# Kernel optimization log

Measured on AMD Instinct MI355X. Metric: run time of the kernel, lower is better.

The kernel has to match this reference:

```python
import jax, jax.numpy as jnp
import numpy as np

HEADS = 8
DIM_HEAD = 64

def setup_inputs() -> dict:
    key = jax.random.key(0)
    k1, k2, k3 = jax.random.split(key, 3)
    B, L, D = 8, 4096, 512
    hidden = HEADS * DIM_HEAD  # 512
    x = jax.random.normal(k1, (B, L, D), dtype=jnp.float32)
    # Conv1d(kernel_size=1) weights, squeezed to 2D matrices
    Wqkv = jax.random.normal(k2, (3 * hidden, D), dtype=jnp.float32) * (1.0 / np.sqrt(D))
    Wout = jax.random.normal(k3, (D, hidden), dtype=jnp.float32) * (1.0 / np.sqrt(hidden))
    bout = jnp.zeros((D,), dtype=jnp.float32)
    return {"x": x, "Wqkv": Wqkv, "Wout": Wout, "bout": bout}

def reference(x, Wqkv, Wout, bout):
    B, L, D = x.shape
    H, C = HEADS, DIM_HEAD
    # pointwise conv == linear over channel dim: (b, 3*H*C, l)
    qkv = jnp.einsum('bld,od->bol', x, Wqkv)
    qkv = qkv.reshape(B, 3, H, C, L)  # channel split order: (qkv, heads, c)
    q, k, v = qkv[:, 0], qkv[:, 1], qkv[:, 2]  # each (b, h, c, l)
    k = jax.nn.softmax(k, axis=-1)   # softmax over sequence
    q = jax.nn.softmax(q, axis=-2)   # softmax over feature dim (q_norm=True)
    context = jnp.einsum('bhdn,bhen->bhde', k, v)   # (b,h,c,c)
    out = jnp.einsum('bhde,bhdn->bhen', context, q)  # (b,h,c,l)
    out = out.reshape(B, H * C, L)
    y = jnp.einsum('bcl,dc->bld', out, Wout) + bout  # to_out + permute back
    return y
```

## Files before the change

kernel.cpp:

```cpp
#include <hip/hip_runtime.h>

#define L 4096
#define D 512
#define NCH 16

typedef __bf16 bf16x8 __attribute__((ext_vector_type(8)));
typedef float  f32x4  __attribute__((ext_vector_type(4)));

__device__ __forceinline__ void load_lds16(const void* g, void* l) {
    __builtin_amdgcn_global_load_lds(
        (const __attribute__((address_space(1))) void*)g,
        (__attribute__((address_space(3))) void*)l, 16, 0, 0);
}

__device__ __forceinline__ void barrier_mem() {
    asm volatile("" ::: "memory");
    __builtin_amdgcn_s_barrier();
    asm volatile("" ::: "memory");
}

#define NX8  (8 * 4096 * 512 / 8)
#define NW18 (1536 * 512 / 8)
#define NW28 (512 * 512 / 8)
__global__ __launch_bounds__(256) void convert_all(const float* __restrict__ x,
                                                   const float* __restrict__ Wq,
                                                   const float* __restrict__ Wo,
                                                   __bf16* __restrict__ dst) {
    int i = blockIdx.x * 256 + threadIdx.x;
    if (i >= NX8 + NW18 + NW28) return;
    const float* s;
    if (i < NX8)             s = x  + (size_t)i * 8;
    else if (i < NX8 + NW18) s = Wq + (size_t)(i - NX8) * 8;
    else                     s = Wo + (size_t)(i - NX8 - NW18) * 8;
    float4 a = ((const float4*)s)[0], b = ((const float4*)s)[1];
    bf16x8 o = {(__bf16)a.x, (__bf16)a.y, (__bf16)a.z, (__bf16)a.w,
                (__bf16)b.x, (__bf16)b.y, (__bf16)b.z, (__bf16)b.w};
    *(bf16x8*)(dst + (size_t)i * 8) = o;
}

template <int M, int N, int K, typename CT>
__global__ __launch_bounds__(512, 2) void gemm_bf16_256(
    const __bf16* __restrict__ A, size_t aStride,
    const __bf16* __restrict__ B, size_t bStride,
    CT* __restrict__ C, size_t cStride,
    const float* __restrict__ bias) {
    __shared__ __align__(16) __bf16 sA[4][256 * 32];
    __shared__ __align__(16) __bf16 sB[4][256 * 32];
    constexpr int NQ = K / 32;
    const int b  = blockIdx.z;
    const int m0 = blockIdx.y * 256;
    const int n0 = blockIdx.x * 256;
    const int t    = threadIdx.x;
    const int wave = t >> 6, lane = t & 63;
    const int wm = (wave >> 2) * 128;
    const int wn = (wave & 3) * 64;
    const int fr = lane & 15, g = lane >> 4;
    const __bf16* Ab = A + (size_t)b * aStride + (size_t)m0 * K;
    const __bf16* Bb = B + (size_t)b * bStride + (size_t)n0 * K;
    CT* Cb = C + (size_t)b * cStride;

    f32x4 acc[8][4];
#pragma unroll
    for (int i = 0; i < 8; i++)
#pragma unroll
        for (int j = 0; j < 4; j++) acc[i][j] = (f32x4)(0.0f);

    auto stageU = [&](const __bf16* Pb, int q, __bf16* slot) {
#pragma unroll
        for (int it = 0; it < 2; ++it) {
            const int gi = it * 512 + t;
            const int row = gi >> 2, cc = gi & 3;
            const int scc = cc ^ ((row >> 1) & 3);
            load_lds16(Pb + (size_t)row * K + q * 32 + scc * 8, slot + gi * 8);
        }
    };
    auto rdFrag = [&](const __bf16* slot, int rowbase) -> bf16x8 {
        const int row = rowbase + fr;
        return *(const bf16x8*)&slot[row * 32 + ((g ^ ((row >> 1) & 3)) * 8)];
    };
    auto readFrags = [&](int sl, bf16x8* fB, bf16x8* fA) {
        const __bf16* sBq = sB[sl];
        const __bf16* sAq = sA[sl];
#pragma unroll
        for (int j = 0; j < 4; ++j) fB[j] = rdFrag(sBq, wn + j * 16);
#pragma unroll
        for (int i = 0; i < 8; ++i) fA[i] = rdFrag(sAq, wm + i * 16);
    };
    auto mfmaAll = [&](const bf16x8* fB, const bf16x8* fA) {
        __builtin_amdgcn_s_setprio(1);
#pragma unroll
        for (int i = 0; i < 8; ++i)
#pragma unroll
            for (int j = 0; j < 4; ++j)
                acc[i][j] = __builtin_amdgcn_mfma_f32_16x16x32_bf16(
                    fA[i], fB[j], acc[i][j], 0, 0, 0);
        __builtin_amdgcn_s_setprio(0);
    };
    auto body = [&](int q, bf16x8* curB, bf16x8* curA, bf16x8* nxtB, bf16x8* nxtA) {
        if (q <= NQ - 3) asm volatile("s_waitcnt vmcnt(8)" ::: "memory");
        else             asm volatile("s_waitcnt vmcnt(0)" ::: "memory");
        barrier_mem();
        if (q + 3 < NQ) {
            stageU(Bb, q + 3, sB[(q + 3) & 3]);
            stageU(Ab, q + 3, sA[(q + 3) & 3]);
        }
        asm volatile("s_waitcnt lgkmcnt(0)" ::: "memory");
        __builtin_amdgcn_sched_barrier(0);
        if (q + 1 < NQ) readFrags((q + 1) & 3, nxtB, nxtA);
        __builtin_amdgcn_sched_barrier(0);
        mfmaAll(curB, curA);
    };

    stageU(Bb, 0, sB[0]); stageU(Ab, 0, sA[0]);
    stageU(Bb, 1, sB[1]); stageU(Ab, 1, sA[1]);
    stageU(Bb, 2, sB[2]); stageU(Ab, 2, sA[2]);
    asm volatile("s_waitcnt vmcnt(16)" ::: "memory");
    barrier_mem();
    bf16x8 fB0[4], fA0[8], fB1[4], fA1[8];
    readFrags(0, fB0, fA0);

    for (int q2 = 0; q2 < NQ; q2 += 2) {
        body(q2,     fB0, fA0, fB1, fA1);
        body(q2 + 1, fB1, fA1, fB0, fA0);
    }

    const int rb = g * 4;
    float bv[4];
#pragma unroll
    for (int j = 0; j < 4; ++j) bv[j] = bias ? bias[n0 + wn + j * 16 + fr] : 0.0f;
#pragma unroll
    for (int i = 0; i < 8; ++i) {
#pragma unroll
        for (int r = 0; r < 4; ++r) {
            const int m = m0 + wm + i * 16 + rb + r;
            CT* rowp = Cb + (size_t)m * N + n0 + wn + fr;
#pragma unroll
            for (int j = 0; j < 4; ++j)
                rowp[j * 16] = (CT)(acc[i][j][r] + bv[j]);
        }
    }
}

__global__ __launch_bounds__(256) void kstats(const __bf16* __restrict__ qkv,
                                              float2* __restrict__ stats) {
    const int r = blockIdx.x;
    const int b = r >> 9, hc = r & 511;
    const __bf16* row = qkv + (size_t)b * 1536 * L + (size_t)(512 + hc) * L;
    __shared__ float sred[4];
    const int t = threadIdx.x;
    const bf16x8* p = (const bf16x8*)row;
    bf16x8 c0 = p[t * 2], c1 = p[t * 2 + 1];
    float v[16];
    float m = -1e30f;
#pragma unroll
    for (int j = 0; j < 8; j++) {
        v[j] = (float)c0[j];
        v[8 + j] = (float)c1[j];
    }
#pragma unroll
    for (int j = 0; j < 16; j++) m = fmaxf(m, v[j]);
#pragma unroll
    for (int off = 32; off > 0; off >>= 1) m = fmaxf(m, __shfl_down(m, off, 64));
    if ((t & 63) == 0) sred[t >> 6] = m;
    __syncthreads();
    const float m4 = fmaxf(fmaxf(sred[0], sred[1]), fmaxf(sred[2], sred[3]));
    float s = 0.f;
#pragma unroll
    for (int j = 0; j < 16; j++) s += __expf(v[j] - m4);
#pragma unroll
    for (int off = 32; off > 0; off >>= 1) s += __shfl_down(s, off, 64);
    __syncthreads();
    if ((t & 63) == 0) sred[t >> 6] = s;
    __syncthreads();
    if (t == 0) {
        const float stot = sred[0] + sred[1] + sred[2] + sred[3];
        stats[r] = make_float2(m4, 1.0f / stot);
    }
}

#define SKS 264
__global__ __launch_bounds__(256) void context_mfma(const __bf16* __restrict__ qkv,
                                                    const float2* __restrict__ stats,
                                                    float* __restrict__ ctxp) {
    __shared__ __align__(16) __bf16 smem[2 * 64 * SKS];
    __shared__ float smax[64];
    __bf16* sk = smem;
    __bf16* sv = smem + 64 * SKS;
    const int chunk = blockIdx.x;
    const int bh = blockIdx.y;
    const int b = bh >> 3, h = bh & 7;
    const __bf16* kbase = qkv + (size_t)b * 1536 * L + (size_t)(512 + h * 64) * L;
    const __bf16* vbase = qkv + (size_t)b * 1536 * L + (size_t)(1024 + h * 64) * L;
    const int t = threadIdx.x;
    if (t < 64) smax[t] = stats[bh * 64 + t].x;
    __syncthreads();

    {
        const int d = t >> 2, noff = (t & 3) * 64;
        const int n0 = chunk * 256;
        const __bf16* kp = kbase + (size_t)d * L + n0 + noff;
        const __bf16* vp = vbase + (size_t)d * L + n0 + noff;
        const float md = smax[d];
#pragma unroll
        for (int c = 0; c < 8; c++) {
            bf16x8 kk = *(const bf16x8*)(kp + c * 8);
            bf16x8 vv = *(const bf16x8*)(vp + c * 8);
            bf16x8 ek;
#pragma unroll
            for (int j = 0; j < 8; j++) ek[j] = (__bf16)__expf((float)kk[j] - md);
            *(bf16x8*)&sk[d * SKS + noff + c * 8] = ek;
            *(bf16x8*)&sv[d * SKS + noff + c * 8] = vv;
        }
    }
    __syncthreads();

    const int wave = t >> 6, lane = t & 63;
    const int fr = lane & 15, kq = (lane >> 4) * 8;
    f32x4 acc[4][4];
#pragma unroll
    for (int i = 0; i < 4; i++)
#pragma unroll
        for (int j = 0; j < 4; j++) acc[i][j] = (f32x4)(0.0f);
#pragma unroll
    for (int kh = 0; kh < 2; kh++) {
        const int koff = wave * 64 + kh * 32 + kq;
        bf16x8 af[4], bfr[4];
#pragma unroll
        for (int i = 0; i < 4; i++) {
            af[i]  = *(const bf16x8*)&sk[(i * 16 + fr) * SKS + koff];
            bfr[i] = *(const bf16x8*)&sv[(i * 16 + fr) * SKS + koff];
        }
#pragma unroll
        for (int i = 0; i < 4; i++)
#pragma unroll
            for (int j = 0; j < 4; j++)
                acc[i][j] = __builtin_amdgcn_mfma_f32_16x16x32_bf16(af[i], bfr[j], acc[i][j], 0, 0, 0);
    }
    __syncthreads();

    float* red = (float*)smem;
    const int col = lane & 15, rbase = (lane >> 4) * 4;
#pragma unroll
    for (int i = 0; i < 4; i++)
#pragma unroll
        for (int j = 0; j < 4; j++)
#pragma unroll
            for (int r = 0; r < 4; r++) {
                const int dd = i * 16 + rbase + r;
                const int ee = j * 16 + col;
                red[wave * 4096 + dd * 64 + ee] = acc[i][j][r];
            }
    __syncthreads();
    float* cp = ctxp + ((size_t)chunk * 64 + bh) * 4096;
#pragma unroll
    for (int gg = 0; gg < 4; gg++) {
        const int idx = t * 16 + gg * 4;
        f32x4 s = *(const f32x4*)&red[idx];
        s += *(const f32x4*)&red[4096 + idx];
        s += *(const f32x4*)&red[8192 + idx];
        s += *(const f32x4*)&red[12288 + idx];
        *(f32x4*)&cp[idx] = s;
    }
}

__global__ __launch_bounds__(256) void ctx_reduce(const float* __restrict__ ctxp,
                                                  const float2* __restrict__ stats,
                                                  __bf16* __restrict__ ctxT) {
    const int bh = blockIdx.x >> 2, quarter = blockIdx.x & 3;
    const int t = threadIdx.x;
    const int flat = quarter * 1024 + t * 4;
    const int d = flat >> 6, e0 = flat & 63;
    f32x4 s = (f32x4)(0.0f);
    for (int ch = 0; ch < NCH; ch++)
        s += *(const f32x4*)&ctxp[((size_t)ch * 64 + bh) * 4096 + flat];
    const float inv = stats[bh * 64 + d].y;
    __bf16* o = ctxT + (size_t)bh * 4096;
#pragma unroll
    for (int j = 0; j < 4; j++) o[(e0 + j) * 64 + d] = (__bf16)(s[j] * inv);
}

#define SPS 66
__global__ __launch_bounds__(256) void pv_fused(__bf16* __restrict__ qkv,
                                                const __bf16* __restrict__ ctxT) {
    __shared__ __align__(16) __bf16 sp[256 * SPS];
    __shared__ __align__(16) __bf16 sctx[64 * SPS];
    __shared__ float sinv[256];
    const int tileN = blockIdx.x;
    const int bh = blockIdx.y;
    const int b = bh >> 3, h = bh & 7;
    const int t = threadIdx.x;
    const int n0 = tileN * 256;
    const __bf16* qbase = qkv + (size_t)b * 1536 * L + (size_t)(h * 64) * L;

    {
        const int e = t >> 2, c = t & 3;
        const bf16x8* src = (const bf16x8*)(ctxT + ((size_t)bh * 64 + e) * 64 + c * 16);
        *(bf16x8*)&sctx[e * SPS + c * 16] = src[0];
        *(bf16x8*)&sctx[e * SPS + c * 16 + 8] = src[1];
    }

    float m = -1e30f;
    float qv[64];
#pragma unroll
    for (int d = 0; d < 64; d++) {
        qv[d] = (float)qbase[(size_t)d * L + n0 + t];
        m = fmaxf(m, qv[d]);
    }
    float s = 0.f;
#pragma unroll
    for (int d0 = 0; d0 < 64; d0 += 8) {
        bf16x8 ek;
#pragma unroll
        for (int j = 0; j < 8; j++) {
            float e = __expf(qv[d0 + j] - m);
            s += e;
            ek[j] = (__bf16)e;
        }
        *(bf16x8*)&sp[t * SPS + d0] = ek;
    }
    sinv[t] = 1.0f / s;
    __syncthreads();

    const int wave = t >> 6, lane = t & 63;
    const int wm = wave * 64;
    const int fr = lane & 15, kq = (lane >> 4) * 8;
    f32x4 acc[4][4];
#pragma unroll
    for (int i = 0; i < 4; i++)
#pragma unroll
        for (int j = 0; j < 4; j++) acc[i][j] = (f32x4)(0.0f);
#pragma unroll
    for (int kh = 0; kh < 2; kh++) {
        bf16x8 af[4], bfr[4];
#pragma unroll
        for (int i = 0; i < 4; i++)
            af[i] = *(const bf16x8*)&sp[(wm + i * 16 + fr) * SPS + kh * 32 + kq];
#pragma unroll
        for (int j = 0; j < 4; j++)
            bfr[j] = *(const bf16x8*)&sctx[(j * 16 + fr) * SPS + kh * 32 + kq];
#pragma unroll
        for (int i = 0; i < 4; i++)
#pragma unroll
            for (int j = 0; j < 4; j++)
                acc[i][j] = __builtin_amdgcn_mfma_f32_16x16x32_bf16(af[i], bfr[j], acc[i][j], 0, 0, 0);
    }

    __bf16* ob = qkv + (size_t)b * 1536 * L + (size_t)512 * L;
    const int col = lane & 15, rbase = (lane >> 4) * 4;
#pragma unroll
    for (int i = 0; i < 4; i++) {
#pragma unroll
        for (int r = 0; r < 4; r++) {
            const int nl = wm + i * 16 + rbase + r;
            const float inv = sinv[nl];
            const size_t rowoff = (size_t)(n0 + nl) * 512 + h * 64;
#pragma unroll
            for (int j = 0; j < 4; j++)
                ob[rowoff + j * 16 + col] = (__bf16)(acc[i][j][r] * inv);
        }
    }
}

extern "C" void kernel_launch(void* const* d_in, const int* in_sizes, int n_in,
                              void* d_out, int out_size, void* d_ws, size_t ws_size,
                              hipStream_t stream) {
    const float* x    = (const float*)d_in[0];
    const float* Wqkv = (const float*)d_in[1];
    const float* Wout = (const float*)d_in[2];
    const float* bout = (const float*)d_in[3];
    float* y = (float*)d_out;

    __bf16* qkv   = (__bf16*)d_ws;
    float*  ctxp  = (float*)(qkv + (size_t)8 * 1536 * L);
    __bf16* xb    = (__bf16*)(ctxp + (size_t)NCH * 64 * 4096);
    __bf16* Wqb   = xb + (size_t)8 * 4096 * 512;
    __bf16* Wob   = Wqb + (size_t)1536 * 512;
    float2* stats = (float2*)(Wob + (size_t)512 * 512);
    __bf16* ctxT  = (__bf16*)(stats + 4096);

    const int convBlocks = (NX8 + NW18 + NW28 + 255) / 256;
    convert_all<<<dim3(convBlocks), 256, 0, stream>>>(x, Wqkv, Wout, xb);

    gemm_bf16_256<1536, 4096, 512, __bf16><<<dim3(4096 / 256, 1536 / 256, 8), 512, 0, stream>>>(
        Wqb, 0, xb, (size_t)4096 * 512, qkv, (size_t)1536 * 4096, nullptr);

    kstats<<<dim3(4096), 256, 0, stream>>>(qkv, stats);
    context_mfma<<<dim3(NCH, 64), 256, 0, stream>>>(qkv, stats, ctxp);
    ctx_reduce<<<dim3(256), 256, 0, stream>>>(ctxp, stats, ctxT);
    pv_fused<<<dim3(L / 256, 64), 256, 0, stream>>>(qkv, ctxT);

    const __bf16* outT = qkv + (size_t)512 * L;
    gemm_bf16_256<4096, 512, 512, float><<<dim3(512 / 256, 4096 / 256, 8), 512, 0, stream>>>(
        outT, (size_t)1536 * L, Wob, 0, y, (size_t)4096 * 512, bout);
}
```

Baseline: 264.3 us.

## Shrink GEMM tile to 256x128 with 4 waves and 3-stage LDS pipeline

Both GEMMs move from a 256x256 tile with 8 waves and a 4-deep LDS ring to a 256x128 tile with 4 waves and a 3-deep ring. The register double-buffering of fragments is dropped: fragments are now read and consumed in the same iteration. The smaller tile doubles the block count and cuts LDS per block, which aims at better occupancy and load balance, especially for the output GEMM (previously only 256 blocks). In exchange, fragment-load latency is no longer hidden behind the previous MFMA batch, and the per-block compute-to-load ratio drops.

```diff
diff --git a/kernel.cpp b/kernel.cpp
--- a/kernel.cpp
+++ b/kernel.cpp
@@ -39,21 +39,21 @@
 }
 
 template <int M, int N, int K, typename CT>
-__global__ __launch_bounds__(512, 2) void gemm_bf16_256(
+__global__ __launch_bounds__(256, 2) void gemm_bf16_256x128(
     const __bf16* __restrict__ A, size_t aStride,
     const __bf16* __restrict__ B, size_t bStride,
     CT* __restrict__ C, size_t cStride,
     const float* __restrict__ bias) {
-    __shared__ __align__(16) __bf16 sA[4][256 * 32];
-    __shared__ __align__(16) __bf16 sB[4][256 * 32];
+    __shared__ __align__(16) __bf16 sA[3][256 * 32];
+    __shared__ __align__(16) __bf16 sB[3][128 * 32];
     constexpr int NQ = K / 32;
     const int b  = blockIdx.z;
     const int m0 = blockIdx.y * 256;
-    const int n0 = blockIdx.x * 256;
+    const int n0 = blockIdx.x * 128;
     const int t    = threadIdx.x;
     const int wave = t >> 6, lane = t & 63;
-    const int wm = (wave >> 2) * 128;
-    const int wn = (wave & 3) * 64;
+    const int wm = (wave >> 1) * 128;
+    const int wn = (wave & 1) * 64;
     const int fr = lane & 15, g = lane >> 4;
     const __bf16* Ab = A + (size_t)b * aStride + (size_t)m0 * K;
     const __bf16* Bb = B + (size_t)b * bStride + (size_t)n0 * K;
@@ -65,28 +65,49 @@
 #pragma unroll
         for (int j = 0; j < 4; j++) acc[i][j] = (f32x4)(0.0f);
 
-    auto stageU = [&](const __bf16* Pb, int q, __bf16* slot) {
-#pragma unroll
-        for (int it = 0; it < 2; ++it) {
-            const int gi = it * 512 + t;
+    auto stageA = [&](int q, __bf16* slot) {
+#pragma unroll
+        for (int it = 0; it < 4; ++it) {
+            const int gi = it * 256 + t;
             const int row = gi >> 2, cc = gi & 3;
             const int scc = cc ^ ((row >> 1) & 3);
-            load_lds16(Pb + (size_t)row * K + q * 32 + scc * 8, slot + gi * 8);
+            load_lds16(Ab + (size_t)row * K + q * 32 + scc * 8, slot + gi * 8);
+        }
+    };
+    auto stageB = [&](int q, __bf16* slot) {
+#pragma unroll
+        for (int it = 0; it < 2; ++it) {
+            const int gi = it * 256 + t;
+            const int row = gi >> 2, cc = gi & 3;
+            const int scc = cc ^ ((row >> 1) & 3);
+            load_lds16(Bb + (size_t)row * K + q * 32 + scc * 8, slot + gi * 8);
         }
     };
     auto rdFrag = [&](const __bf16* slot, int rowbase) -> bf16x8 {
         const int row = rowbase + fr;
         return *(const bf16x8*)&slot[row * 32 + ((g ^ ((row >> 1) & 3)) * 8)];
     };
-    auto readFrags = [&](int sl, bf16x8* fB, bf16x8* fA) {
-        const __bf16* sBq = sB[sl];
-        const __bf16* sAq = sA[sl];
-#pragma unroll
-        for (int j = 0; j < 4; ++j) fB[j] = rdFrag(sBq, wn + j * 16);
-#pragma unroll
-        for (int i = 0; i < 8; ++i) fA[i] = rdFrag(sAq, wm + i * 16);
-    };
-    auto mfmaAll = [&](const bf16x8* fB, const bf16x8* fA) {
+
+    stageB(0, sB[0]); stageA(0, sA[0]);
+    stageB(1, sB[1]); stageA(1, sA[1]);
+
+    for (int q = 0; q < NQ; ++q) {
+        const int sl = q % 3;
+        if (q < NQ - 1) asm volatile("s_waitcnt vmcnt(6)" ::: "memory");
+        else            asm volatile("s_waitcnt vmcnt(0)" ::: "memory");
+        barrier_mem();
+        if (q + 2 < NQ) {
+            const int ss = (q + 2) % 3;
+            stageB(q + 2, sB[ss]);
+            stageA(q + 2, sA[ss]);
+        }
+        bf16x8 fB[4], fA[8];
+#pragma unroll
+        for (int j = 0; j < 4; ++j) fB[j] = rdFrag(sB[sl], wn + j * 16);
+#pragma unroll
+        for (int i = 0; i < 8; ++i) fA[i] = rdFrag(sA[sl], wm + i * 16);
+        asm volatile("s_waitcnt lgkmcnt(0)" ::: "memory");
+        __builtin_amdgcn_sched_barrier(0);
         __builtin_amdgcn_s_setprio(1);
 #pragma unroll
         for (int i = 0; i < 8; ++i)
@@ -95,33 +116,6 @@
                 acc[i][j] = __builtin_amdgcn_mfma_f32_16x16x32_bf16(
                     fA[i], fB[j], acc[i][j], 0, 0, 0);
         __builtin_amdgcn_s_setprio(0);
-    };
-    auto body = [&](int q, bf16x8* curB, bf16x8* curA, bf16x8* nxtB, bf16x8* nxtA) {
-        if (q <= NQ - 3) asm volatile("s_waitcnt vmcnt(8)" ::: "memory");
-        else             asm volatile("s_waitcnt vmcnt(0)" ::: "memory");
-        barrier_mem();
-        if (q + 3 < NQ) {
-            stageU(Bb, q + 3, sB[(q + 3) & 3]);
-            stageU(Ab, q + 3, sA[(q + 3) & 3]);
-        }
-        asm volatile("s_waitcnt lgkmcnt(0)" ::: "memory");
-        __builtin_amdgcn_sched_barrier(0);
-        if (q + 1 < NQ) readFrags((q + 1) & 3, nxtB, nxtA);
-        __builtin_amdgcn_sched_barrier(0);
-        mfmaAll(curB, curA);
-    };
-
-    stageU(Bb, 0, sB[0]); stageU(Ab, 0, sA[0]);
-    stageU(Bb, 1, sB[1]); stageU(Ab, 1, sA[1]);
-    stageU(Bb, 2, sB[2]); stageU(Ab, 2, sA[2]);
-    asm volatile("s_waitcnt vmcnt(16)" ::: "memory");
-    barrier_mem();
-    bf16x8 fB0[4], fA0[8], fB1[4], fA1[8];
-    readFrags(0, fB0, fA0);
-
-    for (int q2 = 0; q2 < NQ; q2 += 2) {
-        body(q2,     fB0, fA0, fB1, fA1);
-        body(q2 + 1, fB1, fA1, fB0, fA0);
     }
 
     const int rb = g * 4;
@@ -381,7 +375,7 @@
     const int convBlocks = (NX8 + NW18 + NW28 + 255) / 256;
     convert_all<<<dim3(convBlocks), 256, 0, stream>>>(x, Wqkv, Wout, xb);
 
-    gemm_bf16_256<1536, 4096, 512, __bf16><<<dim3(4096 / 256, 1536 / 256, 8), 512, 0, stream>>>(
+    gemm_bf16_256x128<1536, 4096, 512, __bf16><<<dim3(4096 / 128, 1536 / 256, 8), 256, 0, stream>>>(
         Wqb, 0, xb, (size_t)4096 * 512, qkv, (size_t)1536 * 4096, nullptr);
 
     kstats<<<dim3(4096), 256, 0, stream>>>(qkv, stats);
@@ -390,6 +384,6 @@
     pv_fused<<<dim3(L / 256, 64), 256, 0, stream>>>(qkv, ctxT);
 
     const __bf16* outT = qkv + (size_t)512 * L;
-    gemm_bf16_256<4096, 512, 512, float><<<dim3(512 / 256, 4096 / 256, 8), 512, 0, stream>>>(
+    gemm_bf16_256x128<4096, 512, 512, float><<<dim3(512 / 128, 4096 / 256, 8), 256, 0, stream>>>(
         outT, (size_t)1536 * L, Wob, 0, y, (size_t)4096 * 512, bout);
 }
```

New measurement: 267.8 us. About the same (+1.3%).
